# Optimization experiments

Hardware: AMD Instinct MI355X
Metric: run time of the kernel (lower is better)

Reference implementation:

```python
import jax, jax.numpy as jnp
import numpy as np

D_MODEL = 1024
HEADS = 16
D_K = D_MODEL // HEADS


def setup_inputs() -> dict:
    key = jax.random.key(0)
    k1, k2, k3, k4, k5 = jax.random.split(key, 5)
    B, S = 4, 2048
    q = jax.random.normal(k1, (B, S, D_MODEL), dtype=jnp.float32)
    # causal mask, broadcastable to [B, H, S, S]; 0 => masked
    mask = jnp.tril(jnp.ones((S, S), dtype=jnp.int32))[None, None, :, :]
    scale = 1.0 / np.sqrt(D_MODEL)
    w_q = jax.random.normal(k2, (D_MODEL, D_MODEL), dtype=jnp.float32) * scale
    w_k = jax.random.normal(k3, (D_MODEL, D_MODEL), dtype=jnp.float32) * scale
    w_v = jax.random.normal(k4, (D_MODEL, D_MODEL), dtype=jnp.float32) * scale
    w_o = jax.random.normal(k5, (D_MODEL, D_MODEL), dtype=jnp.float32) * scale
    return {"q": q, "mask": mask, "w_q": w_q, "w_k": w_k, "w_v": w_v, "w_o": w_o}


def reference(q, mask, w_q, w_k, w_v, w_o):
    B, S, _ = q.shape
    # Linear(bias=False): x @ W^T, then split heads -> [B, H, S, d_k]
    def proj(x, w):
        return (x @ w.T).reshape(B, S, HEADS, D_K).transpose(0, 2, 1, 3)

    Q = proj(q, w_q)
    K = proj(q, w_k)
    V = proj(q, w_v)
    scores = jnp.einsum("bhsd,bhtd->bhst", Q, K) / np.sqrt(D_K)
    scores = jnp.where(mask == 0, jnp.float32(-1e9), scores)
    attn = jax.nn.softmax(scores, axis=-1)  # dropout p=0.0 -> identity
    out = jnp.einsum("bhst,bhtd->bhsd", attn, V)
    out = out.transpose(0, 2, 1, 3).reshape(B, S, D_MODEL)
    return out @ w_o.T
```

## Files before the change

kernel.cpp:

```cpp
#include <hip/hip_runtime.h>
#include <math.h>

#define BATCH 4
#define S_LEN 2048
#define DM    1024
#define NH    16
#define DK    64

typedef __attribute__((ext_vector_type(8))) short short8;
typedef __attribute__((ext_vector_type(4))) float f32x4;

static __device__ __forceinline__ unsigned short bf_hi(float x) {
    union { float f; unsigned u; } c; c.f = x;
    return (unsigned short)(c.u >> 16);
}
static __device__ __forceinline__ float bf_f(unsigned short h) {
    union { unsigned u; float f; } c; c.u = ((unsigned)h) << 16;
    return c.f;
}
static __device__ __forceinline__ unsigned short bf_rnd(float x) {
    union { float f; unsigned u; } c; c.f = x;
    unsigned r = c.u + 0x7fffu + ((c.u >> 16) & 1u);
    return (unsigned short)(r >> 16);
}

template<bool PRESPLIT_A, bool SPLIT_OUT>
__global__ __launch_bounds__(256, 3)
void gemm_k(const float* __restrict__ Af,
            const unsigned short* __restrict__ Agh,
            const unsigned short* __restrict__ Agl,
            const float* __restrict__ W,
            float* __restrict__ Cf,
            unsigned short* __restrict__ Ch,
            unsigned short* __restrict__ Cl,
            float scale, int M, int N, int K)
{
    __shared__ unsigned short Xh[128][40], Xl[128][40];
    __shared__ unsigned short Wh[128][40], Wl[128][40];

    const int tid  = threadIdx.x;
    const int lane = tid & 63;
    const int wid  = tid >> 6;
    const int lrow = lane & 15;
    const int lgrp = lane >> 4;
    const int bm = blockIdx.y * 128;
    const int bn = blockIdx.x * 128;
    const int wm = (wid & 1) * 64;
    const int wn = (wid >> 1) * 64;

    const f32x4 fzero = {0.f, 0.f, 0.f, 0.f};
    f32x4 acc[4][4];
#pragma unroll
    for (int i = 0; i < 4; ++i)
#pragma unroll
        for (int j = 0; j < 4; ++j) acc[i][j] = fzero;

    const int srow = tid >> 2;
    const int sc8  = (tid & 3) * 8;

    for (int kt = 0; kt < K; kt += 32) {
        if constexpr (PRESPLIT_A) {
#pragma unroll
            for (int p = 0; p < 2; ++p) {
                int pos = tid + p * 256;
                int row = pos >> 2;
                int c8  = (pos & 3) * 8;
                *(short8*)&Xh[row][c8] =
                    *(const short8*)(Agh + (size_t)(bm + row) * K + kt + c8);
                *(short8*)&Xl[row][c8] =
                    *(const short8*)(Agl + (size_t)(bm + row) * K + kt + c8);
            }
        } else {
#pragma unroll
            for (int i = 0; i < 2; ++i) {
                const int row = srow + i * 64;
                const float* xp = Af + (size_t)(bm + row) * K + kt + sc8;
                float4 a0 = *(const float4*)xp, a1 = *(const float4*)(xp + 4);
                float va[8] = {a0.x,a0.y,a0.z,a0.w,a1.x,a1.y,a1.z,a1.w};
                short8 xh, xl;
#pragma unroll
                for (int j = 0; j < 8; ++j) {
                    unsigned short h = bf_hi(va[j]);
                    xh[j] = (short)h; xl[j] = (short)bf_hi(va[j] - bf_f(h));
                }
                *(short8*)&Xh[row][sc8] = xh; *(short8*)&Xl[row][sc8] = xl;
            }
        }
#pragma unroll
        for (int i = 0; i < 2; ++i) {
            const int row = srow + i * 64;
            const float* wp = W + (size_t)(bn + row) * K + kt + sc8;
            float4 b0 = *(const float4*)wp, b1 = *(const float4*)(wp + 4);
            float vb[8] = {b0.x,b0.y,b0.z,b0.w,b1.x,b1.y,b1.z,b1.w};
            short8 wh, wl;
#pragma unroll
            for (int j = 0; j < 8; ++j) {
                unsigned short g = bf_hi(vb[j]);
                wh[j] = (short)g; wl[j] = (short)bf_hi(vb[j] - bf_f(g));
            }
            *(short8*)&Wh[row][sc8] = wh; *(short8*)&Wl[row][sc8] = wl;
        }
        __syncthreads();

        short8 ah[4], al[4], bh[4], bl[4];
#pragma unroll
        for (int t = 0; t < 4; ++t) {
            ah[t] = *(const short8*)&Xh[wm + t*16 + lrow][lgrp*8];
            al[t] = *(const short8*)&Xl[wm + t*16 + lrow][lgrp*8];
            bh[t] = *(const short8*)&Wh[wn + t*16 + lrow][lgrp*8];
            bl[t] = *(const short8*)&Wl[wn + t*16 + lrow][lgrp*8];
        }
#pragma unroll
        for (int mt = 0; mt < 4; ++mt)
#pragma unroll
            for (int nt = 0; nt < 4; ++nt) {
                acc[mt][nt] = __builtin_amdgcn_mfma_f32_16x16x32_bf16(ah[mt], bh[nt], acc[mt][nt], 0, 0, 0);
                acc[mt][nt] = __builtin_amdgcn_mfma_f32_16x16x32_bf16(ah[mt], bl[nt], acc[mt][nt], 0, 0, 0);
                acc[mt][nt] = __builtin_amdgcn_mfma_f32_16x16x32_bf16(al[mt], bh[nt], acc[mt][nt], 0, 0, 0);
            }
        __syncthreads();
    }

#pragma unroll
    for (int mt = 0; mt < 4; ++mt)
#pragma unroll
        for (int nt = 0; nt < 4; ++nt)
#pragma unroll
            for (int r = 0; r < 4; ++r) {
                const size_t idx = (size_t)(bm + wm + mt*16 + lgrp*4 + r) * N
                                 + bn + wn + nt*16 + lrow;
                if constexpr (SPLIT_OUT) {
                    float v = acc[mt][nt][r] * scale;
                    unsigned short h = bf_hi(v);
                    Ch[idx] = h;
                    Cl[idx] = bf_hi(v - bf_f(h));
                } else {
                    Cf[idx] = acc[mt][nt][r];
                }
            }
}

__global__ __launch_bounds__(256, 3)
void attn_mfma(const unsigned short* __restrict__ Qh_g, const unsigned short* __restrict__ Ql_g,
               const unsigned short* __restrict__ Kh_g, const unsigned short* __restrict__ Kl_g,
               const unsigned short* __restrict__ Vh_g, const unsigned short* __restrict__ Vl_g,
               unsigned short* __restrict__ Oh_g, unsigned short* __restrict__ Ol_g)
{
    __shared__ unsigned short Ksh[64][72], Ksl[64][72];
    __shared__ unsigned short Vth[64][72], Vtl[64][72];
    __shared__ unsigned short Ps[4][16][72];

    const int tid  = threadIdx.x;
    const int lane = tid & 63;
    const int wid  = tid >> 6;
    const int lrow = lane & 15;
    const int lgrp = lane >> 4;

    const int rt = (int)(gridDim.x - 1u - blockIdx.x);
    const int bh = blockIdx.y;
    const int b  = bh >> 4;
    const int h  = bh & 15;

    const size_t base = (size_t)b * S_LEN * DM + (size_t)h * DK;
    const int row0 = rt * 64;

    short8 qh[2], ql[2];
#pragma unroll
    for (int c = 0; c < 2; ++c) {
        const size_t qoff = base + (size_t)(row0 + wid*16 + lrow) * DM + c*32 + lgrp*8;
        qh[c] = *(const short8*)(Qh_g + qoff);
        ql[c] = *(const short8*)(Ql_g + qoff);
    }

    const f32x4 fzero = {0.f, 0.f, 0.f, 0.f};
    f32x4 o[4];
    float m[4], l[4];
#pragma unroll
    for (int i = 0; i < 4; ++i) { o[i] = fzero; m[i] = -1e30f; l[i] = 0.f; }

    const int skey = tid >> 3;
    const int sc8  = (tid & 7) * 8;
    const int vk0  = (tid >> 4) * 4;
    const int vd0  = (tid & 15) * 4;

    for (int kt = 0; kt <= rt; ++kt) {
        const size_t kb = base + (size_t)(kt * 64) * DM;

#pragma unroll
        for (int i = 0; i < 2; ++i) {
            const int key = skey + i * 32;
            const size_t off = kb + (size_t)key * DM + sc8;
            *(short8*)&Ksh[key][sc8] = *(const short8*)(Kh_g + off);
            *(short8*)&Ksl[key][sc8] = *(const short8*)(Kl_g + off);
        }
        {
            ushort4 ah4[4], al4[4];
#pragma unroll
            for (int kk = 0; kk < 4; ++kk) {
                const size_t off = kb + (size_t)(vk0 + kk) * DM + vd0;
                ah4[kk] = *(const ushort4*)(Vh_g + off);
                al4[kk] = *(const ushort4*)(Vl_g + off);
            }
#pragma unroll
            for (int j = 0; j < 4; ++j) {
                const unsigned short* e0 = (const unsigned short*)&ah4[0];
                const unsigned short* e1 = (const unsigned short*)&ah4[1];
                const unsigned short* e2 = (const unsigned short*)&ah4[2];
                const unsigned short* e3 = (const unsigned short*)&ah4[3];
                uint2 wh, wl;
                wh.x = (unsigned)e0[j] | ((unsigned)e1[j] << 16);
                wh.y = (unsigned)e2[j] | ((unsigned)e3[j] << 16);
                const unsigned short* f0 = (const unsigned short*)&al4[0];
                const unsigned short* f1 = (const unsigned short*)&al4[1];
                const unsigned short* f2 = (const unsigned short*)&al4[2];
                const unsigned short* f3 = (const unsigned short*)&al4[3];
                wl.x = (unsigned)f0[j] | ((unsigned)f1[j] << 16);
                wl.y = (unsigned)f2[j] | ((unsigned)f3[j] << 16);
                *(uint2*)&Vth[vd0 + j][vk0] = wh;
                *(uint2*)&Vtl[vd0 + j][vk0] = wl;
            }
        }
        __syncthreads();

        f32x4 s[4];
#pragma unroll
        for (int t = 0; t < 4; ++t) s[t] = fzero;
#pragma unroll
        for (int t = 0; t < 4; ++t)
#pragma unroll
            for (int c = 0; c < 2; ++c) {
                short8 kh = *(const short8*)&Ksh[t*16 + lrow][c*32 + lgrp*8];
                short8 kl = *(const short8*)&Ksl[t*16 + lrow][c*32 + lgrp*8];
                s[t] = __builtin_amdgcn_mfma_f32_16x16x32_bf16(qh[c], kh, s[t], 0, 0, 0);
                s[t] = __builtin_amdgcn_mfma_f32_16x16x32_bf16(ql[c], kh, s[t], 0, 0, 0);
                s[t] = __builtin_amdgcn_mfma_f32_16x16x32_bf16(qh[c], kl, s[t], 0, 0, 0);
            }

        if (kt == rt) {
            const int qloc = wid * 16 + lgrp * 4;
#pragma unroll
            for (int t = 0; t < 4; ++t)
#pragma unroll
                for (int r = 0; r < 4; ++r)
                    if (t*16 + lrow > qloc + r) s[t][r] = -1e30f;
        }

        float pm[4];
#pragma unroll
        for (int r = 0; r < 4; ++r)
            pm[r] = fmaxf(fmaxf(s[0][r], s[1][r]), fmaxf(s[2][r], s[3][r]));
#pragma unroll
        for (int off = 8; off >= 1; off >>= 1)
#pragma unroll
            for (int r = 0; r < 4; ++r)
                pm[r] = fmaxf(pm[r], __shfl_xor(pm[r], off));

        float rs[4], rowsum[4];
#pragma unroll
        for (int r = 0; r < 4; ++r) {
            float mn = fmaxf(m[r], pm[r]);
            rs[r] = __expf(m[r] - mn);
            m[r] = mn;
            rowsum[r] = 0.f;
        }
#pragma unroll
        for (int t = 0; t < 4; ++t)
#pragma unroll
            for (int r = 0; r < 4; ++r) {
                float p = __expf(s[t][r] - m[r]);
                s[t][r] = p;
                rowsum[r] += p;
            }
#pragma unroll
        for (int off = 8; off >= 1; off >>= 1)
#pragma unroll
            for (int r = 0; r < 4; ++r)
                rowsum[r] += __shfl_xor(rowsum[r], off);
#pragma unroll
        for (int r = 0; r < 4; ++r) l[r] = l[r] * rs[r] + rowsum[r];
#pragma unroll
        for (int dt = 0; dt < 4; ++dt)
#pragma unroll
            for (int r = 0; r < 4; ++r) o[dt][r] *= rs[r];

#pragma unroll
        for (int t = 0; t < 4; ++t)
#pragma unroll
            for (int r = 0; r < 4; ++r)
                Ps[wid][lgrp*4 + r][t*16 + lrow] = bf_rnd(s[t][r]);

#pragma unroll
        for (int kc = 0; kc < 2; ++kc) {
            short8 pa = *(const short8*)&Ps[wid][lrow][kc*32 + lgrp*8];
#pragma unroll
            for (int dt = 0; dt < 4; ++dt) {
                short8 vh = *(const short8*)&Vth[dt*16 + lrow][kc*32 + lgrp*8];
                short8 vl = *(const short8*)&Vtl[dt*16 + lrow][kc*32 + lgrp*8];
                o[dt] = __builtin_amdgcn_mfma_f32_16x16x32_bf16(pa, vh, o[dt], 0, 0, 0);
                o[dt] = __builtin_amdgcn_mfma_f32_16x16x32_bf16(pa, vl, o[dt], 0, 0, 0);
            }
        }
        __syncthreads();
    }

#pragma unroll
    for (int r = 0; r < 4; ++r) {
        float inv = 1.f / l[r];
#pragma unroll
        for (int dt = 0; dt < 4; ++dt) {
            const size_t idx = base + (size_t)(row0 + wid*16 + lgrp*4 + r) * DM + dt*16 + lrow;
            float v = o[dt][r] * inv;
            unsigned short hh = bf_hi(v);
            Oh_g[idx] = hh;
            Ol_g[idx] = bf_hi(v - bf_f(hh));
        }
    }
}

extern "C" void kernel_launch(void* const* d_in, const int* in_sizes, int n_in,
                              void* d_out, int out_size, void* d_ws, size_t ws_size,
                              hipStream_t stream)
{
    const float* q   = (const float*)d_in[0];
    const float* w_q = (const float*)d_in[2];
    const float* w_k = (const float*)d_in[3];
    const float* w_v = (const float*)d_in[4];
    const float* w_o = (const float*)d_in[5];
    float* out = (float*)d_out;

    const size_t HN = (size_t)BATCH * S_LEN * DM;
    unsigned short* Qh = (unsigned short*)d_ws;
    unsigned short* Ql = Qh + HN;
    unsigned short* Kh = Ql + HN;
    unsigned short* Kl = Kh + HN;
    unsigned short* Vh = Kl + HN;
    unsigned short* Vl = Vh + HN;
    unsigned short* Oh = Qh;
    unsigned short* Ol = Ql;

    const int M = BATCH * S_LEN;
    dim3 blk(256);
    dim3 ggrid(DM / 128, M / 128);
    gemm_k<false, true><<<ggrid, blk, 0, stream>>>(q, nullptr, nullptr, w_q,
                                                   nullptr, Qh, Ql, 0.125f, M, DM, DM);
    gemm_k<false, true><<<ggrid, blk, 0, stream>>>(q, nullptr, nullptr, w_k,
                                                   nullptr, Kh, Kl, 1.0f, M, DM, DM);
    gemm_k<false, true><<<ggrid, blk, 0, stream>>>(q, nullptr, nullptr, w_v,
                                                   nullptr, Vh, Vl, 1.0f, M, DM, DM);

    dim3 agrid(S_LEN / 64, BATCH * NH);
    attn_mfma<<<agrid, blk, 0, stream>>>(Qh, Ql, Kh, Kl, Vh, Vl, Oh, Ol);

    gemm_k<true, false><<<ggrid, blk, 0, stream>>>(nullptr, Oh, Ol, w_o,
                                                   out, nullptr, nullptr, 1.0f, M, DM, DM);
}
```

Measured before the change: 756.6 us.

## Enlarge attention query tile to 128 rows and register-prefetch next K/V tile

Each attention block now processes 128 query rows (two 16-row subtiles per wave) instead of 64, so every K/V tile loaded into shared memory serves twice as many queries and global K/V traffic is halved. The next K/V tile is loaded into registers while the current tile is being computed, overlapping global loads with MFMA work. Subtiles that lie entirely above the causal diagonal are skipped. The cost is higher register pressure, which may lower occupancy under launch_bounds(256,3), and the grid has half as many blocks, leaving less parallelism and coarser causal load balancing.

```diff
diff --git a/kernel.cpp b/kernel.cpp
--- a/kernel.cpp
+++ b/kernel.cpp
@@ -156,165 +156,202 @@
     const int lrow = lane & 15;
     const int lgrp = lane >> 4;
 
-    const int rt = (int)(gridDim.x - 1u - blockIdx.x);
+    const int qb = (int)(gridDim.x - 1u - blockIdx.x);
     const int bh = blockIdx.y;
     const int b  = bh >> 4;
     const int h  = bh & 15;
 
     const size_t base = (size_t)b * S_LEN * DM + (size_t)h * DK;
-    const int row0 = rt * 64;
-
-    short8 qh[2], ql[2];
-#pragma unroll
-    for (int c = 0; c < 2; ++c) {
-        const size_t qoff = base + (size_t)(row0 + wid*16 + lrow) * DM + c*32 + lgrp*8;
-        qh[c] = *(const short8*)(Qh_g + qoff);
-        ql[c] = *(const short8*)(Ql_g + qoff);
-    }
+    const int row0  = qb * 128;
+    const int ktmax = 2 * qb + 1;
+
+    short8 qh[2][2], ql[2][2];
+#pragma unroll
+    for (int rt = 0; rt < 2; ++rt)
+#pragma unroll
+        for (int c = 0; c < 2; ++c) {
+            const size_t qoff = base + (size_t)(row0 + wid*32 + rt*16 + lrow) * DM
+                              + c*32 + lgrp*8;
+            qh[rt][c] = *(const short8*)(Qh_g + qoff);
+            ql[rt][c] = *(const short8*)(Ql_g + qoff);
+        }
 
     const f32x4 fzero = {0.f, 0.f, 0.f, 0.f};
-    f32x4 o[4];
-    float m[4], l[4];
-#pragma unroll
-    for (int i = 0; i < 4; ++i) { o[i] = fzero; m[i] = -1e30f; l[i] = 0.f; }
+    f32x4 o[2][4];
+    float m[2][4], l[2][4];
+#pragma unroll
+    for (int rt = 0; rt < 2; ++rt)
+#pragma unroll
+        for (int i = 0; i < 4; ++i) { o[rt][i] = fzero; m[rt][i] = -1e30f; l[rt][i] = 0.f; }
 
     const int skey = tid >> 3;
     const int sc8  = (tid & 7) * 8;
     const int vk0  = (tid >> 4) * 4;
     const int vd0  = (tid & 15) * 4;
 
-    for (int kt = 0; kt <= rt; ++kt) {
-        const size_t kb = base + (size_t)(kt * 64) * DM;
-
+    short8  pkh[2], pkl[2];
+    ushort4 pvh[4], pvl[4];
+
+    {
+        const size_t kb = base;
 #pragma unroll
         for (int i = 0; i < 2; ++i) {
-            const int key = skey + i * 32;
-            const size_t off = kb + (size_t)key * DM + sc8;
-            *(short8*)&Ksh[key][sc8] = *(const short8*)(Kh_g + off);
-            *(short8*)&Ksl[key][sc8] = *(const short8*)(Kl_g + off);
-        }
-        {
-            ushort4 ah4[4], al4[4];
+            const size_t off = kb + (size_t)(skey + i*32) * DM + sc8;
+            pkh[i] = *(const short8*)(Kh_g + off);
+            pkl[i] = *(const short8*)(Kl_g + off);
+        }
+#pragma unroll
+        for (int kk = 0; kk < 4; ++kk) {
+            const size_t off = kb + (size_t)(vk0 + kk) * DM + vd0;
+            pvh[kk] = *(const ushort4*)(Vh_g + off);
+            pvl[kk] = *(const ushort4*)(Vl_g + off);
+        }
+    }
+
+    for (int kt = 0; kt <= ktmax; ++kt) {
+#pragma unroll
+        for (int i = 0; i < 2; ++i) {
+            *(short8*)&Ksh[skey + i*32][sc8] = pkh[i];
+            *(short8*)&Ksl[skey + i*32][sc8] = pkl[i];
+        }
+#pragma unroll
+        for (int j = 0; j < 4; ++j) {
+            const unsigned short* e0 = (const unsigned short*)&pvh[0];
+            const unsigned short* e1 = (const unsigned short*)&pvh[1];
+            const unsigned short* e2 = (const unsigned short*)&pvh[2];
+            const unsigned short* e3 = (const unsigned short*)&pvh[3];
+            uint2 wh, wl;
+            wh.x = (unsigned)e0[j] | ((unsigned)e1[j] << 16);
+            wh.y = (unsigned)e2[j] | ((unsigned)e3[j] << 16);
+            const unsigned short* f0 = (const unsigned short*)&pvl[0];
+            const unsigned short* f1 = (const unsigned short*)&pvl[1];
+            const unsigned short* f2 = (const unsigned short*)&pvl[2];
+            const unsigned short* f3 = (const unsigned short*)&pvl[3];
+            wl.x = (unsigned)f0[j] | ((unsigned)f1[j] << 16);
+            wl.y = (unsigned)f2[j] | ((unsigned)f3[j] << 16);
+            *(uint2*)&Vth[vd0 + j][vk0] = wh;
+            *(uint2*)&Vtl[vd0 + j][vk0] = wl;
+        }
+        __syncthreads();
+
+        if (kt < ktmax) {
+            const size_t kb = base + (size_t)((kt + 1) * 64) * DM;
+#pragma unroll
+            for (int i = 0; i < 2; ++i) {
+                const size_t off = kb + (size_t)(skey + i*32) * DM + sc8;
+                pkh[i] = *(const short8*)(Kh_g + off);
+                pkl[i] = *(const short8*)(Kl_g + off);
+            }
 #pragma unroll
             for (int kk = 0; kk < 4; ++kk) {
                 const size_t off = kb + (size_t)(vk0 + kk) * DM + vd0;
-                ah4[kk] = *(const ushort4*)(Vh_g + off);
-                al4[kk] = *(const ushort4*)(Vl_g + off);
-            }
-#pragma unroll
-            for (int j = 0; j < 4; ++j) {
-                const unsigned short* e0 = (const unsigned short*)&ah4[0];
-                const unsigned short* e1 = (const unsigned short*)&ah4[1];
-                const unsigned short* e2 = (const unsigned short*)&ah4[2];
-                const unsigned short* e3 = (const unsigned short*)&ah4[3];
-                uint2 wh, wl;
-                wh.x = (unsigned)e0[j] | ((unsigned)e1[j] << 16);
-                wh.y = (unsigned)e2[j] | ((unsigned)e3[j] << 16);
-                const unsigned short* f0 = (const unsigned short*)&al4[0];
-                const unsigned short* f1 = (const unsigned short*)&al4[1];
-                const unsigned short* f2 = (const unsigned short*)&al4[2];
-                const unsigned short* f3 = (const unsigned short*)&al4[3];
-                wl.x = (unsigned)f0[j] | ((unsigned)f1[j] << 16);
-                wl.y = (unsigned)f2[j] | ((unsigned)f3[j] << 16);
-                *(uint2*)&Vth[vd0 + j][vk0] = wh;
-                *(uint2*)&Vtl[vd0 + j][vk0] = wl;
-            }
-        }
-        __syncthreads();
-
-        f32x4 s[4];
-#pragma unroll
-        for (int t = 0; t < 4; ++t) s[t] = fzero;
-#pragma unroll
-        for (int t = 0; t < 4; ++t)
-#pragma unroll
-            for (int c = 0; c < 2; ++c) {
-                short8 kh = *(const short8*)&Ksh[t*16 + lrow][c*32 + lgrp*8];
-                short8 kl = *(const short8*)&Ksl[t*16 + lrow][c*32 + lgrp*8];
-                s[t] = __builtin_amdgcn_mfma_f32_16x16x32_bf16(qh[c], kh, s[t], 0, 0, 0);
-                s[t] = __builtin_amdgcn_mfma_f32_16x16x32_bf16(ql[c], kh, s[t], 0, 0, 0);
-                s[t] = __builtin_amdgcn_mfma_f32_16x16x32_bf16(qh[c], kl, s[t], 0, 0, 0);
-            }
-
-        if (kt == rt) {
-            const int qloc = wid * 16 + lgrp * 4;
+                pvh[kk] = *(const ushort4*)(Vh_g + off);
+                pvl[kk] = *(const ushort4*)(Vl_g + off);
+            }
+        }
+
+#pragma unroll
+        for (int rt = 0; rt < 2; ++rt) {
+            const int qbase = wid * 32 + rt * 16;
+            if (kt * 64 > row0 + qbase + 15) continue;
+
+            f32x4 s[4];
+#pragma unroll
+            for (int t = 0; t < 4; ++t) s[t] = fzero;
 #pragma unroll
             for (int t = 0; t < 4; ++t)
 #pragma unroll
+                for (int c = 0; c < 2; ++c) {
+                    short8 kh = *(const short8*)&Ksh[t*16 + lrow][c*32 + lgrp*8];
+                    short8 kl = *(const short8*)&Ksl[t*16 + lrow][c*32 + lgrp*8];
+                    s[t] = __builtin_amdgcn_mfma_f32_16x16x32_bf16(qh[rt][c], kh, s[t], 0, 0, 0);
+                    s[t] = __builtin_amdgcn_mfma_f32_16x16x32_bf16(ql[rt][c], kh, s[t], 0, 0, 0);
+                    s[t] = __builtin_amdgcn_mfma_f32_16x16x32_bf16(qh[rt][c], kl, s[t], 0, 0, 0);
+                }
+
+            if (kt * 64 + 63 > row0 + qbase) {
+#pragma unroll
+                for (int t = 0; t < 4; ++t)
+#pragma unroll
+                    for (int r = 0; r < 4; ++r)
+                        if (kt*64 + t*16 + lrow > row0 + qbase + lgrp*4 + r)
+                            s[t][r] = -1e30f;
+            }
+
+            float pm[4];
+#pragma unroll
+            for (int r = 0; r < 4; ++r)
+                pm[r] = fmaxf(fmaxf(s[0][r], s[1][r]), fmaxf(s[2][r], s[3][r]));
+#pragma unroll
+            for (int off = 8; off >= 1; off >>= 1)
+#pragma unroll
                 for (int r = 0; r < 4; ++r)
-                    if (t*16 + lrow > qloc + r) s[t][r] = -1e30f;
-        }
-
-        float pm[4];
-#pragma unroll
-        for (int r = 0; r < 4; ++r)
-            pm[r] = fmaxf(fmaxf(s[0][r], s[1][r]), fmaxf(s[2][r], s[3][r]));
-#pragma unroll
-        for (int off = 8; off >= 1; off >>= 1)
-#pragma unroll
-            for (int r = 0; r < 4; ++r)
-                pm[r] = fmaxf(pm[r], __shfl_xor(pm[r], off));
-
-        float rs[4], rowsum[4];
-#pragma unroll
-        for (int r = 0; r < 4; ++r) {
-            float mn = fmaxf(m[r], pm[r]);
-            rs[r] = __expf(m[r] - mn);
-            m[r] = mn;
-            rowsum[r] = 0.f;
-        }
-#pragma unroll
-        for (int t = 0; t < 4; ++t)
+                    pm[r] = fmaxf(pm[r], __shfl_xor(pm[r], off));
+
+            float rs[4], rowsum[4];
 #pragma unroll
             for (int r = 0; r < 4; ++r) {
-                float p = __expf(s[t][r] - m[r]);
-                s[t][r] = p;
-                rowsum[r] += p;
-            }
-#pragma unroll
-        for (int off = 8; off >= 1; off >>= 1)
-#pragma unroll
-            for (int r = 0; r < 4; ++r)
-                rowsum[r] += __shfl_xor(rowsum[r], off);
-#pragma unroll
-        for (int r = 0; r < 4; ++r) l[r] = l[r] * rs[r] + rowsum[r];
-#pragma unroll
-        for (int dt = 0; dt < 4; ++dt)
-#pragma unroll
-            for (int r = 0; r < 4; ++r) o[dt][r] *= rs[r];
-
-#pragma unroll
-        for (int t = 0; t < 4; ++t)
-#pragma unroll
-            for (int r = 0; r < 4; ++r)
-                Ps[wid][lgrp*4 + r][t*16 + lrow] = bf_rnd(s[t][r]);
-
-#pragma unroll
-        for (int kc = 0; kc < 2; ++kc) {
-            short8 pa = *(const short8*)&Ps[wid][lrow][kc*32 + lgrp*8];
-#pragma unroll
-            for (int dt = 0; dt < 4; ++dt) {
-                short8 vh = *(const short8*)&Vth[dt*16 + lrow][kc*32 + lgrp*8];
-                short8 vl = *(const short8*)&Vtl[dt*16 + lrow][kc*32 + lgrp*8];
-                o[dt] = __builtin_amdgcn_mfma_f32_16x16x32_bf16(pa, vh, o[dt], 0, 0, 0);
-                o[dt] = __builtin_amdgcn_mfma_f32_16x16x32_bf16(pa, vl, o[dt], 0, 0, 0);
+                float mn = fmaxf(m[rt][r], pm[r]);
+                rs[r] = __expf(m[rt][r] - mn);
+                m[rt][r] = mn;
+                rowsum[r] = 0.f;
+            }
+#pragma unroll
+            for (int t = 0; t < 4; ++t)
+#pragma unroll
+                for (int r = 0; r < 4; ++r) {
+                    float p = __expf(s[t][r] - m[rt][r]);
+                    s[t][r] = p;
+                    rowsum[r] += p;
+                }
+#pragma unroll
+            for (int off = 8; off >= 1; off >>= 1)
+#pragma unroll
+                for (int r = 0; r < 4; ++r)
+                    rowsum[r] += __shfl_xor(rowsum[r], off);
+#pragma unroll
+            for (int r = 0; r < 4; ++r) l[rt][r] = l[rt][r] * rs[r] + rowsum[r];
+#pragma unroll
+            for (int dt = 0; dt < 4; ++dt)
+#pragma unroll
+                for (int r = 0; r < 4; ++r) o[rt][dt][r] *= rs[r];
+
+#pragma unroll
+            for (int t = 0; t < 4; ++t)
+#pragma unroll
+                for (int r = 0; r < 4; ++r)
+                    Ps[wid][lgrp*4 + r][t*16 + lrow] = bf_rnd(s[t][r]);
+
+#pragma unroll
+            for (int kc = 0; kc < 2; ++kc) {
+                short8 pa = *(const short8*)&Ps[wid][lrow][kc*32 + lgrp*8];
+#pragma unroll
+                for (int dt = 0; dt < 4; ++dt) {
+                    short8 vh = *(const short8*)&Vth[dt*16 + lrow][kc*32 + lgrp*8];
+                    short8 vl = *(const short8*)&Vtl[dt*16 + lrow][kc*32 + lgrp*8];
+                    o[rt][dt] = __builtin_amdgcn_mfma_f32_16x16x32_bf16(pa, vh, o[rt][dt], 0, 0, 0);
+                    o[rt][dt] = __builtin_amdgcn_mfma_f32_16x16x32_bf16(pa, vl, o[rt][dt], 0, 0, 0);
+                }
             }
         }
         __syncthreads();
     }
 
 #pragma unroll
-    for (int r = 0; r < 4; ++r) {
-        float inv = 1.f / l[r];
-#pragma unroll
-        for (int dt = 0; dt < 4; ++dt) {
-            const size_t idx = base + (size_t)(row0 + wid*16 + lgrp*4 + r) * DM + dt*16 + lrow;
-            float v = o[dt][r] * inv;
-            unsigned short hh = bf_hi(v);
-            Oh_g[idx] = hh;
-            Ol_g[idx] = bf_hi(v - bf_f(hh));
-        }
-    }
+    for (int rt = 0; rt < 2; ++rt)
+#pragma unroll
+        for (int r = 0; r < 4; ++r) {
+            float inv = 1.f / l[rt][r];
+#pragma unroll
+            for (int dt = 0; dt < 4; ++dt) {
+                const size_t idx = base
+                    + (size_t)(row0 + wid*32 + rt*16 + lgrp*4 + r) * DM + dt*16 + lrow;
+                float v = o[rt][dt][r] * inv;
+                unsigned short hh = bf_hi(v);
+                Oh_g[idx] = hh;
+                Ol_g[idx] = bf_hi(v - bf_f(hh));
+            }
+        }
 }
 
 extern "C" void kernel_launch(void* const* d_in, const int* in_sizes, int n_in,
@@ -348,7 +385,7 @@
     gemm_k<false, true><<<ggrid, blk, 0, stream>>>(q, nullptr, nullptr, w_v,
                                                    nullptr, Vh, Vl, 1.0f, M, DM, DM);
 
-    dim3 agrid(S_LEN / 64, BATCH * NH);
+    dim3 agrid(S_LEN / 128, BATCH * NH);
     attn_mfma<<<agrid, blk, 0, stream>>>(Qh, Ql, Kh, Kl, Vh, Vl, Oh, Ol);
 
     gemm_k<true, false><<<ggrid, blk, 0, stream>>>(nullptr, Oh, Ol, w_o,
```

Measured after the change: 843.3 us. 11.5% more time.
